# Kernel optimization log

Hardware: AMD Instinct MI355X
Metric: run time of the kernel (lower is better)

## Reference

```python
import jax, jax.numpy as jnp
import numpy as np

B, S, D, H, F = 2, 2048, 1024, 16, 4096
HD = D // H
EPS = 1e-5


def _layernorm(x, g, b):
    mu = jnp.mean(x, axis=-1, keepdims=True)
    var = jnp.var(x, axis=-1, keepdims=True)
    return (x - mu) * jax.lax.rsqrt(var + EPS) * g + b


def setup_inputs() -> dict:
    key = jax.random.key(0)
    ks = jax.random.split(key, 10)
    sd = 0.02
    return {
        "src": jax.random.normal(ks[0], (B, S, D), jnp.float32),
        "qkv_w": jax.random.normal(ks[1], (3 * D, D), jnp.float32) * sd,
        "qkv_b": jnp.zeros((3 * D,), jnp.float32),
        "out_w": jax.random.normal(ks[2], (D, D), jnp.float32) * sd,
        "out_b": jnp.zeros((D,), jnp.float32),
        "ffn_w1": jax.random.normal(ks[3], (F, D), jnp.float32) * sd,
        "ffn_b1": jnp.zeros((F,), jnp.float32),
        "ffn_w2": jax.random.normal(ks[4], (D, F), jnp.float32) * sd,
        "ffn_b2": jnp.zeros((D,), jnp.float32),
        "ln1_g": jnp.ones((D,), jnp.float32),
        "ln1_b": jnp.zeros((D,), jnp.float32),
        "ln2_g": jnp.ones((D,), jnp.float32),
        "ln2_b": jnp.zeros((D,), jnp.float32),
    }


def reference(src, qkv_w, qkv_b, out_w, out_b, ffn_w1, ffn_b1, ffn_w2, ffn_b2,
              ln1_g, ln1_b, ln2_g, ln2_b):
    # --- Multi-head self-attention (post-norm, dropout=identity in eval) ---
    qkv = src @ qkv_w.T + qkv_b                        # [B,S,3D]
    qkv = qkv.reshape(B, S, H, 3 * HD).transpose(0, 2, 1, 3)  # [B,H,S,3hd]
    q, k, v = jnp.split(qkv, 3, axis=-1)               # each [B,H,S,hd]
    scores = jnp.einsum('bhqd,bhkd->bhqk', q, k) / np.sqrt(HD).astype(np.float32)
    attn = jax.nn.softmax(scores, axis=-1)
    ctx = jnp.einsum('bhqk,bhkd->bhqd', attn, v)       # [B,H,S,hd]
    ctx = ctx.transpose(0, 2, 1, 3).reshape(B, S, D)
    mha_out = ctx @ out_w.T + out_b
    agg = _layernorm(src + mha_out, ln1_g, ln1_b)
    # --- FFN: Linear -> ReLU -> Linear ---
    h = jax.nn.relu(agg @ ffn_w1.T + ffn_b1)
    ffn_out = h @ ffn_w2.T + ffn_b2
    return _layernorm(agg + ffn_out, ln2_g, ln2_b)
```

## Files before the change

### kernel.cpp

```cpp
#include <hip/hip_runtime.h>


typedef unsigned short u16;
typedef unsigned int u32;
typedef __attribute__((ext_vector_type(8))) __bf16 bf16x8;
typedef __attribute__((ext_vector_type(4))) float f32x4;
typedef __attribute__((ext_vector_type(4))) short s16x4;
typedef __attribute__((ext_vector_type(2))) u32 u32x2;

__device__ __forceinline__ u16 f2bf(float f) {
  u32 u = __float_as_uint(f);
  u += 0x7fffu + ((u >> 16) & 1u);
  return (u16)(u >> 16);
}

__device__ __forceinline__ float bf2f(u16 h) {
  return __uint_as_float((u32)h << 16);
}

__device__ __forceinline__ u32 pk_bf_trunc(float a, float b) {
  return (__float_as_uint(a) >> 16) | (__float_as_uint(b) & 0xffff0000u);
}

__device__ __forceinline__ float exp2_fast(float x) {
  float t = __builtin_fmaf(x, 8388608.0f, 1064992506.0f);
  return __int_as_float((int)t);
}

__device__ __forceinline__ void async16(const void* g, void* l) {
  __builtin_amdgcn_global_load_lds((__attribute__((address_space(1))) void*)g,
                                   (__attribute__((address_space(3))) void*)l,
                                   16, 0, 0);
}

__device__ __forceinline__ f32x4 mfma16(bf16x8 a, bf16x8 b, f32x4 c) {
  return __builtin_amdgcn_mfma_f32_16x16x32_bf16(a, b, c, 0, 0, 0);
}

__device__ __forceinline__ f32x4 mfma_pv(s16x4 a, s16x4 b, f32x4 c) {
#if __has_builtin(__builtin_amdgcn_mfma_f32_16x16x16bf16_1k)
  return __builtin_amdgcn_mfma_f32_16x16x16bf16_1k(a, b, c, 0, 0, 0);
#else
  f32x4 d;
  asm("v_mfma_f32_16x16x16_bf16 %0, %1, %2, %3" : "=v"(d) : "v"(a), "v"(b), "v"(c));
  return d;
#endif
}

__global__ __launch_bounds__(256)
void cvt_all(const float* __restrict__ qkv_w, const float* __restrict__ out_w,
             const float* __restrict__ f1, const float* __restrict__ f2,
             const float* __restrict__ src,
             u16* __restrict__ o_qkv, u16* __restrict__ o_out,
             u16* __restrict__ o_f1, u16* __restrict__ o_f2,
             u16* __restrict__ o_src) {
  int b = blockIdx.x;
  const float* in;
  u16* out;
  int lb, ob;
  if (b < 3072) {
    int h = b / 192, c = b - h * 192;
    ob = (c < 64) ? h * 64 + c : (c < 128) ? 1024 + h * 64 + (c - 64)
                                           : 2048 + h * 64 + (c - 128);
    in = qkv_w; out = o_qkv; lb = b;
  }
  else if (b < 4096)  { in = out_w; out = o_out; lb = b - 3072;  ob = lb; }
  else if (b < 8192)  { in = f1;    out = o_f1;  lb = b - 4096;  ob = lb; }
  else if (b < 12288) { in = f2;    out = o_f2;  lb = b - 8192;  ob = lb; }
  else                { in = src;   out = o_src; lb = b - 12288; ob = lb; }
  int i = lb * 256 + threadIdx.x;
  int o = ob * 256 + threadIdx.x;
  float4 v = ((const float4*)in)[i];
  ushort4 ov;
  ov.x = f2bf(v.x); ov.y = f2bf(v.y); ov.z = f2bf(v.z); ov.w = f2bf(v.w);
  ((ushort4*)out)[o] = ov;
}

template <int MODE, int SPLIT>
__global__ __launch_bounds__(256)
void gemm_bt(const u16* __restrict__ A, const u16* __restrict__ W,
             const float* __restrict__ bias,
             u16* __restrict__ outb,
             u16* __restrict__ qo, u16* __restrict__ ko, u16* __restrict__ vto,
             int M, int N, int K) {
  __shared__ u16 As[128 * 64];
  __shared__ u16 Bs[128 * 64];
  const int lane = threadIdx.x & 63;
  const int wave = threadIdx.x >> 6;
  const int lrow = lane & 15;
  const int lq = lane >> 4;
  const int tm = blockIdx.x * 128;
  const int tn = blockIdx.y * 128;
  const int wm = (wave >> 1) * 64;
  const int wn = (wave & 1) * 64;
  const int kc = K / SPLIT;
  const int kbeg = blockIdx.z * kc;
  f32x4 acc[4][4] = {};

  for (int k0 = kbeg; k0 < kbeg + kc; k0 += 64) {
#pragma unroll
    for (int c = 0; c < 4; ++c) {
      int chunk = wave * 256 + c * 64 + lane;
      int row = chunk >> 3;
      int sc = chunk & 7;
      int cc = sc ^ (row & 7);
      u16* la = As + (size_t)(wave * 256 + c * 64) * 8;
      u16* lb = Bs + (size_t)(wave * 256 + c * 64) * 8;
      async16(A + (size_t)(tm + row) * K + (k0 + cc * 8), la);
      async16(W + (size_t)(tn + row) * K + (k0 + cc * 8), lb);
    }
    __syncthreads();
#pragma unroll
    for (int h = 0; h < 2; ++h) {
      bf16x8 a_frag[4], b_frag[4];
#pragma unroll
      for (int i = 0; i < 4; ++i) {
        int row = wm + i * 16 + lrow;
        int sc = (h * 4 + lq) ^ (row & 7);
        a_frag[i] = *(const bf16x8*)(As + row * 64 + sc * 8);
      }
#pragma unroll
      for (int j = 0; j < 4; ++j) {
        int row = wn + j * 16 + lrow;
        int sc = (h * 4 + lq) ^ (row & 7);
        b_frag[j] = *(const bf16x8*)(Bs + row * 64 + sc * 8);
      }
#pragma unroll
      for (int i = 0; i < 4; ++i)
#pragma unroll
        for (int j = 0; j < 4; ++j)
          acc[i][j] = mfma16(a_frag[i], b_frag[j], acc[i][j]);
    }
    __syncthreads();
  }

  u16* outp = outb;
  if constexpr (MODE == 0) outp += (size_t)blockIdx.z * M * N;

#pragma unroll
  for (int i = 0; i < 4; ++i) {
#pragma unroll
    for (int j = 0; j < 4; ++j) {
      int col = tn + wn + j * 16 + lrow;
      float bv = (SPLIT == 1 || blockIdx.z == 0) ? bias[col] : 0.f;
#pragma unroll
      for (int r = 0; r < 4; ++r) {
        int row = tm + wm + i * 16 + lq * 4 + r;
        float v = acc[i][j][r] + bv;
        if constexpr (MODE == 0) {
          outp[(size_t)row * N + col] = f2bf(v);
        } else {
          outp[(size_t)row * N + col] = f2bf(fmaxf(v, 0.f));
        }
      }
    }
  }
}

template <int MODE, int SPLIT>
__global__ __launch_bounds__(512, 2)
void gemm8p(const u16* __restrict__ A, const u16* __restrict__ W,
            const float* __restrict__ bias, u16* __restrict__ outb,
            u16* __restrict__ qo, u16* __restrict__ ko, u16* __restrict__ vto,
            int N, int Kfull) {
  extern __shared__ u16 lds[];
  constexpr int NTK = 16;
  constexpr int NG = NTK / 2;
  u16* As = lds;
  u16* Bs = lds + 32768;
  const int tid = threadIdx.x;
  const int lane = tid & 63;
  const int wave = tid >> 6;
  const int lrow = lane & 15;
  const int lq = lane >> 4;
  const int wm = wave >> 2;
  const int wn = wave & 3;
  const int kbeg = blockIdx.y * 1024;

  const int nwg = gridDim.x;
  const int wg = blockIdx.x;
  const int swz = (wg & 7) * (nwg >> 3) + (wg >> 3);
  const int tm = (swz & 15) * 256;
  const int tn = (swz >> 4) * 256;

  auto stage = [&](const u16* __restrict__ T, int trow0, int kt, int rbase,
                   u16* base) {
#pragma unroll
    for (int it = 0; it < 2; ++it) {
      int c = it * 512 + tid;
      int row = c >> 3, sc = c & 7, cc = sc ^ (row & 7);
      async16(T + (size_t)(trow0 + rbase + row) * Kfull + kbeg + kt * 64 + cc * 8,
              base + rbase * 64 + (it * 512 + wave * 64) * 8);
    }
  };
  auto ldA = [&](int buf, int m, int h) {
    int row = wm * 128 + m * 16 + lrow;
    int sc = (h * 4 + lq) ^ (row & 7);
    return *(const bf16x8*)(As + buf * 16384 + row * 64 + sc * 8);
  };
  auto ldB = [&](int buf, int n, int h) {
    int row = wn * 64 + n * 16 + lrow;
    int sc = (h * 4 + lq) ^ (row & 7);
    return *(const bf16x8*)(Bs + buf * 16384 + row * 64 + sc * 8);
  };

  f32x4 acc[8][4] = {};
  bf16x8 a[4][2], b[4][2];

  stage(A, tm, 0, 0, As);
  stage(A, tm, 0, 128, As);
  stage(W, tn, 0, 0, Bs);
  stage(W, tn, 0, 128, Bs);
  stage(W, tn, 1, 0, Bs + 16384);
  stage(A, tm, 1, 0, As + 16384);
  asm volatile("s_waitcnt vmcnt(4)" ::: "memory");
  __builtin_amdgcn_s_barrier();

  for (int g = 0; g < NG; ++g) {
    const int t = 2 * g;
    const int t1k = t + 1;
    const int t2k = (t + 2 < NTK) ? t + 2 : NTK - 1;
    const int t3k = (t + 3 < NTK) ? t + 3 : NTK - 1;

#pragma unroll
    for (int m = 0; m < 4; ++m) { a[m][0] = ldA(0, m, 0); a[m][1] = ldA(0, m, 1); }
#pragma unroll
    for (int n = 0; n < 2; ++n) { b[n][0] = ldB(0, n, 0); b[n][1] = ldB(0, n, 1); }
    stage(A, tm, t1k, 128, As + 16384);
    __builtin_amdgcn_s_barrier();
    asm volatile("s_waitcnt lgkmcnt(0)" ::: "memory");
    __builtin_amdgcn_s_setprio(1);
#pragma unroll
    for (int m = 0; m < 4; ++m)
#pragma unroll
      for (int n = 0; n < 2; ++n) {
        acc[m][n] = mfma16(a[m][0], b[n][0], acc[m][n]);
        acc[m][n] = mfma16(a[m][1], b[n][1], acc[m][n]);
      }
    __builtin_amdgcn_s_setprio(0);
    __builtin_amdgcn_s_barrier();

#pragma unroll
    for (int n = 0; n < 2; ++n) { b[2 + n][0] = ldB(0, 2 + n, 0); b[2 + n][1] = ldB(0, 2 + n, 1); }
    stage(W, tn, t1k, 128, Bs + 16384);
    __builtin_amdgcn_s_barrier();
    asm volatile("s_waitcnt lgkmcnt(0)" ::: "memory");
    __builtin_amdgcn_s_setprio(1);
#pragma unroll
    for (int m = 0; m < 4; ++m)
#pragma unroll
      for (int n = 0; n < 2; ++n) {
        acc[m][2 + n] = mfma16(a[m][0], b[2 + n][0], acc[m][2 + n]);
        acc[m][2 + n] = mfma16(a[m][1], b[2 + n][1], acc[m][2 + n]);
      }
    __builtin_amdgcn_s_setprio(0);
    __builtin_amdgcn_s_barrier();

#pragma unroll
    for (int m = 0; m < 4; ++m) { a[m][0] = ldA(0, 4 + m, 0); a[m][1] = ldA(0, 4 + m, 1); }
    stage(W, tn, t2k, 0, Bs);
    __builtin_amdgcn_s_barrier();
    asm volatile("s_waitcnt lgkmcnt(0)" ::: "memory");
    __builtin_amdgcn_s_setprio(1);
#pragma unroll
    for (int m = 0; m < 4; ++m)
#pragma unroll
      for (int n = 0; n < 2; ++n) {
        acc[4 + m][n] = mfma16(a[m][0], b[n][0], acc[4 + m][n]);
        acc[4 + m][n] = mfma16(a[m][1], b[n][1], acc[4 + m][n]);
      }
    __builtin_amdgcn_s_setprio(0);
    __builtin_amdgcn_s_barrier();

    stage(A, tm, t2k, 0, As);
    asm volatile("s_waitcnt vmcnt(4)" ::: "memory");
    __builtin_amdgcn_s_barrier();
    __builtin_amdgcn_s_setprio(1);
#pragma unroll
    for (int m = 0; m < 4; ++m)
#pragma unroll
      for (int n = 0; n < 2; ++n) {
        acc[4 + m][2 + n] = mfma16(a[m][0], b[2 + n][0], acc[4 + m][2 + n]);
        acc[4 + m][2 + n] = mfma16(a[m][1], b[2 + n][1], acc[4 + m][2 + n]);
      }
    __builtin_amdgcn_s_setprio(0);
    __builtin_amdgcn_s_barrier();

#pragma unroll
    for (int m = 0; m < 4; ++m) { a[m][0] = ldA(1, m, 0); a[m][1] = ldA(1, m, 1); }
#pragma unroll
    for (int n = 0; n < 2; ++n) { b[n][0] = ldB(1, n, 0); b[n][1] = ldB(1, n, 1); }
    stage(A, tm, t2k, 128, As);
    __builtin_amdgcn_s_barrier();
    asm volatile("s_waitcnt lgkmcnt(0)" ::: "memory");
    __builtin_amdgcn_s_setprio(1);
#pragma unroll
    for (int m = 0; m < 4; ++m)
#pragma unroll
      for (int n = 0; n < 2; ++n) {
        acc[m][n] = mfma16(a[m][0], b[n][0], acc[m][n]);
        acc[m][n] = mfma16(a[m][1], b[n][1], acc[m][n]);
      }
    __builtin_amdgcn_s_setprio(0);
    __builtin_amdgcn_s_barrier();

#pragma unroll
    for (int n = 0; n < 2; ++n) { b[2 + n][0] = ldB(1, 2 + n, 0); b[2 + n][1] = ldB(1, 2 + n, 1); }
    stage(W, tn, t2k, 128, Bs);
    __builtin_amdgcn_s_barrier();
    asm volatile("s_waitcnt lgkmcnt(0)" ::: "memory");
    __builtin_amdgcn_s_setprio(1);
#pragma unroll
    for (int m = 0; m < 4; ++m)
#pragma unroll
      for (int n = 0; n < 2; ++n) {
        acc[m][2 + n] = mfma16(a[m][0], b[2 + n][0], acc[m][2 + n]);
        acc[m][2 + n] = mfma16(a[m][1], b[2 + n][1], acc[m][2 + n]);
      }
    __builtin_amdgcn_s_setprio(0);
    __builtin_amdgcn_s_barrier();

#pragma unroll
    for (int m = 0; m < 4; ++m) { a[m][0] = ldA(1, 4 + m, 0); a[m][1] = ldA(1, 4 + m, 1); }
    stage(W, tn, t3k, 0, Bs + 16384);
    __builtin_amdgcn_s_barrier();
    asm volatile("s_waitcnt lgkmcnt(0)" ::: "memory");
    __builtin_amdgcn_s_setprio(1);
#pragma unroll
    for (int m = 0; m < 4; ++m)
#pragma unroll
      for (int n = 0; n < 2; ++n) {
        acc[4 + m][n] = mfma16(a[m][0], b[n][0], acc[4 + m][n]);
        acc[4 + m][n] = mfma16(a[m][1], b[n][1], acc[4 + m][n]);
      }
    __builtin_amdgcn_s_setprio(0);
    __builtin_amdgcn_s_barrier();

    stage(A, tm, t3k, 0, As + 16384);
    asm volatile("s_waitcnt vmcnt(4)" ::: "memory");
    __builtin_amdgcn_s_barrier();
    __builtin_amdgcn_s_setprio(1);
#pragma unroll
    for (int m = 0; m < 4; ++m)
#pragma unroll
      for (int n = 0; n < 2; ++n) {
        acc[4 + m][2 + n] = mfma16(a[m][0], b[2 + n][0], acc[4 + m][2 + n]);
        acc[4 + m][2 + n] = mfma16(a[m][1], b[2 + n][1], acc[4 + m][2 + n]);
      }
    __builtin_amdgcn_s_setprio(0);
    __builtin_amdgcn_s_barrier();
  }
  asm volatile("s_waitcnt vmcnt(0)" ::: "memory");

  if constexpr (MODE == 0) {
    u16* outp = outb + (size_t)blockIdx.y * 4096 * N;
#pragma unroll
    for (int m = 0; m < 8; ++m)
#pragma unroll
      for (int n = 0; n < 4; ++n) {
        int col = tn + wn * 64 + n * 16 + lrow;
        float bv = (SPLIT == 1 || blockIdx.y == 0) ? bias[col] : 0.f;
#pragma unroll
        for (int r = 0; r < 4; ++r) {
          int row = tm + wm * 128 + m * 16 + lq * 4 + r;
          outp[(size_t)row * N + col] = f2bf(acc[m][n][r] + bv);
        }
      }
  } else if constexpr (MODE == 1) {
#pragma unroll
    for (int m = 0; m < 8; ++m)
#pragma unroll
      for (int n = 0; n < 4; ++n) {
        int col = tn + wn * 64 + n * 16 + lrow;
        float bv = bias[col];
#pragma unroll
        for (int r = 0; r < 4; ++r) {
          int row = tm + wm * 128 + m * 16 + lq * 4 + r;
          outb[(size_t)row * N + col] = f2bf(fmaxf(acc[m][n][r] + bv, 0.f));
        }
      }
  } else {
    const int type = tn >> 10;
    if (type < 2) {
      u16* dst = (type == 0) ? qo : ko;
      const float scale = (type == 0) ? 0.1803368801f : 1.f;
#pragma unroll
      for (int n = 0; n < 4; ++n) {
        int idx = (tn & 1023) + wn * 64 + n * 16 + lrow;
        int hh = idx >> 6, c = idx & 63;
        float bv = bias[hh * 192 + type * 64 + c];
#pragma unroll
        for (int m = 0; m < 8; ++m) {
#pragma unroll
          for (int r = 0; r < 4; ++r) {
            int row = tm + wm * 128 + m * 16 + lq * 4 + r;
            int bb = row >> 11, s = row & 2047;
            dst[(((size_t)(bb * 16 + hh) * 2048 + s) << 6) + c] =
                f2bf((acc[m][n][r] + bv) * scale);
          }
        }
      }
    } else {
#pragma unroll
      for (int n = 0; n < 4; ++n) {
        int idx = (tn & 1023) + wn * 64 + n * 16 + lrow;
        int hh = idx >> 6, c = idx & 63;
        float bv = bias[hh * 192 + 128 + c];
#pragma unroll
        for (int m = 0; m < 8; ++m) {
          int row0 = tm + wm * 128 + m * 16 + lq * 4;
          int bb = row0 >> 11, s0 = row0 & 2047;
          ushort4 pk;
          pk.x = f2bf(acc[m][n][0] + bv);
          pk.y = f2bf(acc[m][n][1] + bv);
          pk.z = f2bf(acc[m][n][2] + bv);
          pk.w = f2bf(acc[m][n][3] + bv);
          *(ushort4*)(vto + (((size_t)(bb * 16 + hh) * 64 + c) << 11) + s0) = pk;
        }
      }
    }
  }
}

__global__ __launch_bounds__(512)
void attn_kernel(const u16* __restrict__ Q, const u16* __restrict__ K,
                 const u16* __restrict__ Vt,
                 u16* __restrict__ o_part, float* __restrict__ l_part) {
  extern __shared__ u16 smem[];
  u16* Ks = smem;
  u16* Vs = smem + 16384;
  const int tid = threadIdx.x;
  const int lane = tid & 63;
  const int wave = tid >> 6;
  const int wq = wave & 3;
  const int role = wave >> 2;
  const int lrow = lane & 15;
  const int q = lane >> 4;
  const int bh = blockIdx.x & 31;
  const int qb = (blockIdx.x >> 5) & 7;
  const int kvh = blockIdx.x >> 8;
  const u16* Qp = Q + ((size_t)bh * 2048 + qb * 256) * 64;
  const u16* Kp = K + (size_t)bh * 2048 * 64;
  const u16* Vp = Vt + (size_t)bh * 64 * 2048;

  bf16x8 qf[2][2];
#pragma unroll
  for (int h2 = 0; h2 < 2; ++h2)
#pragma unroll
    for (int kk = 0; kk < 2; ++kk)
      qf[h2][kk] = *(const bf16x8*)(Qp + (h2 * 128 + wave * 16 + lrow) * 64 +
                                    kk * 32 + q * 8);

  const s16x4 ones = {(short)0x3F80, (short)0x3F80, (short)0x3F80, (short)0x3F80};
  f32x4 oacc[2][4] = {};
  f32x4 lacc[2] = {};

  auto stage = [&](int kb, int buf) {
    if (role == 0) {
#pragma unroll
      for (int t = 0; t < 4; ++t) {
        int c = wq * 256 + t * 64 + lane;
        int row = c >> 3, sc = c & 7;
        int cc = sc ^ (row & 7);
        async16(Kp + (size_t)(kb * 128 + row) * 64 + cc * 8,
                Ks + buf * 8192 + (size_t)(wq * 256 + t * 64) * 8);
      }
    } else {
#pragma unroll
      for (int t = 0; t < 4; ++t) {
        int c = wq * 256 + t * 64 + lane;
        int row = c >> 4, sc = c & 15;
        int cc = sc ^ (row & 7);
        async16(Vp + (size_t)row * 2048 + kb * 128 + cc * 8,
                Vs + buf * 8192 + (size_t)(wq * 256 + t * 64) * 8);
      }
    }
  };

  const int kb0 = kvh * 8;
  stage(kb0, 0);
  asm volatile("s_waitcnt vmcnt(0)" ::: "memory");
  __builtin_amdgcn_s_barrier();

  for (int i = 0; i < 8; ++i) {
    const int buf = i & 1;
    if (i < 7) stage(kb0 + i + 1, buf ^ 1);
    const u16* Kb = Ks + buf * 8192;
    const u16* Vb = Vs + buf * 8192;

#pragma unroll
    for (int h2 = 0; h2 < 2; ++h2) {
      f32x4 sacc[8] = {};
#pragma unroll
      for (int j = 0; j < 8; ++j) {
#pragma unroll
        for (int kk = 0; kk < 2; ++kk) {
          int row = j * 16 + lrow;
          int sc = (kk * 4 + q) ^ (row & 7);
          bf16x8 kf = *(const bf16x8*)(Kb + row * 64 + sc * 8);
          sacc[j] = mfma16(kf, qf[h2][kk], sacc[j]);
        }
      }

      s16x4 pa[8];
#pragma unroll
      for (int j = 0; j < 8; ++j) {
        float p0 = exp2_fast(sacc[j][0]);
        float p1 = exp2_fast(sacc[j][1]);
        float p2 = exp2_fast(sacc[j][2]);
        float p3 = exp2_fast(sacc[j][3]);
        u32x2 pw;
        pw.x = pk_bf_trunc(p0, p1);
        pw.y = pk_bf_trunc(p2, p3);
        pa[j] = __builtin_bit_cast(s16x4, pw);
      }

#pragma unroll
      for (int j = 0; j < 8; ++j) {
        lacc[h2] = mfma_pv(pa[j], ones, lacc[h2]);
#pragma unroll
        for (int jn = 0; jn < 4; ++jn) {
          int row = jn * 16 + lrow;
          int sc = (j * 2 + (q >> 1)) ^ (row & 7);
          s16x4 vb = *(const s16x4*)(Vb + row * 128 + sc * 8 + (q & 1) * 4);
          oacc[h2][jn] = mfma_pv(pa[j], vb, oacc[h2][jn]);
        }
      }
    }

    if (i < 7) {
      asm volatile("s_waitcnt vmcnt(0)" ::: "memory");
      __builtin_amdgcn_s_barrier();
    }
  }

  const int b = bh >> 4, h = bh & 15;
  u16* op = o_part + (size_t)kvh * 4096 * 1024;
  float* lp = l_part + kvh * 65536 + bh * 2048;
#pragma unroll
  for (int h2 = 0; h2 < 2; ++h2) {
#pragma unroll
    for (int r = 0; r < 4; ++r) {
      int s = qb * 256 + h2 * 128 + wave * 16 + q * 4 + r;
      if (lrow == 0) lp[s] = lacc[h2][r];
      size_t base = ((size_t)(b * 2048 + s)) * 1024 + h * 64;
#pragma unroll
      for (int jn = 0; jn < 4; ++jn)
        op[base + jn * 16 + lrow] = f2bf(oacc[h2][jn][r]);
    }
  }
}

__global__ __launch_bounds__(256)
void attn_combine(const u16* __restrict__ o_part, const float* __restrict__ l_part,
                  u16* __restrict__ ctx) {
  const int t = blockIdx.x;
  const int tid = threadIdx.x;
  __shared__ float linv[16];
  if (tid < 16) {
    int b = t >> 11, s = t & 2047;
    int bh = b * 16 + tid;
    linv[tid] = 1.f / (l_part[bh * 2048 + s] + l_part[65536 + bh * 2048 + s]);
  }
  __syncthreads();
  size_t base = (size_t)t * 1024;
  ushort4 a = ((const ushort4*)(o_part + base))[tid];
  ushort4 c = ((const ushort4*)(o_part + 4096ull * 1024 + base))[tid];
  float li = linv[tid >> 4];
  ushort4 o;
  o.x = f2bf((bf2f(a.x) + bf2f(c.x)) * li);
  o.y = f2bf((bf2f(a.y) + bf2f(c.y)) * li);
  o.z = f2bf((bf2f(a.z) + bf2f(c.z)) * li);
  o.w = f2bf((bf2f(a.w) + bf2f(c.w)) * li);
  ((ushort4*)(ctx + base))[tid] = o;
}

template <int P>
__global__ __launch_bounds__(256)
void ln_kernel(const float* __restrict__ x1, const u16* __restrict__ x2,
               const float* __restrict__ g, const float* __restrict__ bb,
               float* __restrict__ outf, u16* __restrict__ outb) {
  const int t = blockIdx.x;
  const int tid = threadIdx.x;
  const int lane = tid & 63, wave = tid >> 6;
  const size_t base = (size_t)t * 1024;
  const size_t pstride = 4096ull * 1024;
  float v[4];
  float s = 0.f, s2 = 0.f;
#pragma unroll
  for (int e = 0; e < 4; ++e) {
    int i = tid + e * 256;
    float x = x1[base + i];
#pragma unroll
    for (int p = 0; p < P; ++p) x += bf2f(x2[p * pstride + base + i]);
    v[e] = x;
    s += x;
    s2 += x * x;
  }
#pragma unroll
  for (int d = 1; d < 64; d <<= 1) {
    s += __shfl_xor(s, d);
    s2 += __shfl_xor(s2, d);
  }
  __shared__ float red[8];
  if (lane == 0) { red[wave] = s; red[4 + wave] = s2; }
  __syncthreads();
  s = red[0] + red[1] + red[2] + red[3];
  s2 = red[4] + red[5] + red[6] + red[7];
  float mean = s * (1.f / 1024.f);
  float var = s2 * (1.f / 1024.f) - mean * mean;
  float rstd = rsqrtf(var + 1e-5f);
#pragma unroll
  for (int e = 0; e < 4; ++e) {
    int i = tid + e * 256;
    float y = (v[e] - mean) * rstd * g[i] + bb[i];
    outf[base + i] = y;
    if (outb) outb[base + i] = f2bf(y);
  }
}

extern "C" void kernel_launch(void* const* d_in, const int* in_sizes, int n_in,
                              void* d_out, int out_size, void* d_ws, size_t ws_size,
                              hipStream_t stream) {
  const float* src    = (const float*)d_in[0];
  const float* qkv_w  = (const float*)d_in[1];
  const float* qkv_b  = (const float*)d_in[2];
  const float* out_w  = (const float*)d_in[3];
  const float* out_b  = (const float*)d_in[4];
  const float* ffn_w1 = (const float*)d_in[5];
  const float* ffn_b1 = (const float*)d_in[6];
  const float* ffn_w2 = (const float*)d_in[7];
  const float* ffn_b2 = (const float*)d_in[8];
  const float* ln1_g  = (const float*)d_in[9];
  const float* ln1_b  = (const float*)d_in[10];
  const float* ln2_g  = (const float*)d_in[11];
  const float* ln2_b  = (const float*)d_in[12];

  char* ws = (char*)d_ws;
  size_t off = 0;
  auto alloc = [&](size_t bytes) -> void* {
    void* p = ws + off;
    off += (bytes + 255) & ~(size_t)255;
    return p;
  };
  u16* wqkv = (u16*)alloc(3072ull * 1024 * 2);
  u16* wout = (u16*)alloc(1024ull * 1024 * 2);
  u16* wf1  = (u16*)alloc(4096ull * 1024 * 2);
  u16* wf2  = (u16*)alloc(1024ull * 4096 * 2);
  u16* srcb = (u16*)alloc(4096ull * 1024 * 2);
  u16* qb_  = (u16*)alloc(32ull * 2048 * 64 * 2);
  u16* kb_  = (u16*)alloc(32ull * 2048 * 64 * 2);
  u16* vtb  = (u16*)alloc(32ull * 64 * 2048 * 2);
  u16* opart = (u16*)alloc(2ull * 4096 * 1024 * 2);
  float* lpart = (float*)alloc(2ull * 65536 * 4);
  u16* ctxb = (u16*)alloc(4096ull * 1024 * 2);
  u16* mha  = (u16*)alloc(4ull * 4096 * 1024 * 2);
  float* aggf = (float*)alloc(4096ull * 1024 * 4);
  u16* aggb = (u16*)alloc(4096ull * 1024 * 2);
  u16* hb   = (u16*)alloc(4096ull * 4096 * 2);
  u16* ffnf = (u16*)alloc(4ull * 4096 * 1024 * 2);

  static bool attr_done = false;
  if (!attr_done) {
    auto* kq = gemm8p<2, 1>;
    auto* kf = gemm8p<1, 1>;
    auto* k2 = gemm8p<0, 4>;
    hipFuncSetAttribute(reinterpret_cast<const void*>(kq),
                        hipFuncAttributeMaxDynamicSharedMemorySize, 131072);
    hipFuncSetAttribute(reinterpret_cast<const void*>(kf),
                        hipFuncAttributeMaxDynamicSharedMemorySize, 131072);
    hipFuncSetAttribute(reinterpret_cast<const void*>(k2),
                        hipFuncAttributeMaxDynamicSharedMemorySize, 131072);
    hipFuncSetAttribute(reinterpret_cast<const void*>(attn_kernel),
                        hipFuncAttributeMaxDynamicSharedMemorySize, 65536);
    attr_done = true;
  }

  cvt_all<<<16384, 256, 0, stream>>>(qkv_w, out_w, ffn_w1, ffn_w2, src,
                                     wqkv, wout, wf1, wf2, srcb);

  gemm8p<2, 1><<<dim3(192, 1), 512, 131072, stream>>>(srcb, wqkv, qkv_b, nullptr,
                                                      qb_, kb_, vtb, 3072, 1024);
  attn_kernel<<<512, 512, 65536, stream>>>(qb_, kb_, vtb, opart, lpart);
  attn_combine<<<4096, 256, 0, stream>>>(opart, lpart, ctxb);
  gemm_bt<0, 4><<<dim3(32, 8, 4), 256, 0, stream>>>(ctxb, wout, out_b, mha,
                                                    nullptr, nullptr, nullptr, 4096, 1024, 1024);
  ln_kernel<4><<<4096, 256, 0, stream>>>(src, mha, ln1_g, ln1_b, aggf, aggb);
  gemm8p<1, 1><<<dim3(256, 1), 512, 131072, stream>>>(aggb, wf1, ffn_b1, hb,
                                                      nullptr, nullptr, nullptr, 4096, 1024);
  gemm8p<0, 4><<<dim3(64, 4), 512, 131072, stream>>>(hb, wf2, ffn_b2, ffnf,
                                                     nullptr, nullptr, nullptr, 1024, 4096);
  ln_kernel<4><<<4096, 256, 0, stream>>>(aggf, ffnf, ln2_g, ln2_b, (float*)d_out, nullptr);
}
```

Measured before the change: 362.8 us.

## Transpose V epilogue through LDS and share V fragment loads across query halves

In the QKV GEMM epilogue, the transposed V output is now staged through a per-wave LDS tile so each lane writes 16-byte contiguous chunks along the sequence dimension, replacing scattered 8-byte stores. A barrier is added before the epilogue so the LDS can be reused safely. In the attention kernel, the P fragments for both query halves are computed first, and each V fragment read from LDS then feeds both halves' PV MFMAs, halving V LDS reads. The cost is higher register pressure from holding both P arrays, plus extra LDS waits in the epilogue.

```diff
diff --git a/kernel.cpp b/kernel.cpp
--- a/kernel.cpp
+++ b/kernel.cpp
@@ -351,6 +351,7 @@
     __builtin_amdgcn_s_barrier();
   }
   asm volatile("s_waitcnt vmcnt(0)" ::: "memory");
+  __builtin_amdgcn_s_barrier();
 
   if constexpr (MODE == 0) {
     u16* outp = outb + (size_t)blockIdx.y * 4096 * N;
@@ -401,21 +402,36 @@
         }
       }
     } else {
-#pragma unroll
-      for (int n = 0; n < 4; ++n) {
-        int idx = (tn & 1023) + wn * 64 + n * 16 + lrow;
-        int hh = idx >> 6, c = idx & 63;
-        float bv = bias[hh * 192 + 128 + c];
-#pragma unroll
-        for (int m = 0; m < 8; ++m) {
-          int row0 = tm + wm * 128 + m * 16 + lq * 4;
-          int bb = row0 >> 11, s0 = row0 & 2047;
-          ushort4 pk;
-          pk.x = f2bf(acc[m][n][0] + bv);
-          pk.y = f2bf(acc[m][n][1] + bv);
-          pk.z = f2bf(acc[m][n][2] + bv);
-          pk.w = f2bf(acc[m][n][3] + bv);
-          *(ushort4*)(vto + (((size_t)(bb * 16 + hh) * 64 + c) << 11) + s0) = pk;
+      u16* T = lds + wave * 640;
+      const int bb = tm >> 11;
+      const int s_base = (tm & 2047) + wm * 128;
+      const int idxl = lane & 15, sg = lane >> 4;
+      const int idx2 = (tn & 1023) + wn * 64 + idxl;
+#pragma unroll
+      for (int p = 0; p < 4; ++p) {
+#pragma unroll
+        for (int n = 0; n < 4; ++n) {
+          int idx = (tn & 1023) + wn * 64 + n * 16 + lrow;
+          int hh = idx >> 6, c = idx & 63;
+          float bv = bias[hh * 192 + 128 + c];
+          ushort4 lo, hi;
+          lo.x = f2bf(acc[2 * p][n][0] + bv);
+          lo.y = f2bf(acc[2 * p][n][1] + bv);
+          lo.z = f2bf(acc[2 * p][n][2] + bv);
+          lo.w = f2bf(acc[2 * p][n][3] + bv);
+          hi.x = f2bf(acc[2 * p + 1][n][0] + bv);
+          hi.y = f2bf(acc[2 * p + 1][n][1] + bv);
+          hi.z = f2bf(acc[2 * p + 1][n][2] + bv);
+          hi.w = f2bf(acc[2 * p + 1][n][3] + bv);
+          *(ushort4*)(T + lrow * 40 + lq * 4) = lo;
+          *(ushort4*)(T + lrow * 40 + 16 + lq * 4) = hi;
+          asm volatile("s_waitcnt lgkmcnt(0)" ::: "memory");
+          int i2 = idx2 + n * 16;
+          int hh2 = i2 >> 6, c2 = i2 & 63;
+          uint4 v = *(const uint4*)(T + idxl * 40 + sg * 8);
+          *(uint4*)(vto + (((size_t)(bb * 16 + hh2) * 64 + c2) << 11)
+                        + s_base + p * 32 + sg * 8) = v;
+          asm volatile("s_waitcnt lgkmcnt(0)" ::: "memory");
         }
       }
     }
@@ -488,6 +504,7 @@
     const u16* Kb = Ks + buf * 8192;
     const u16* Vb = Vs + buf * 8192;
 
+    s16x4 pa2[2][8];
 #pragma unroll
     for (int h2 = 0; h2 < 2; ++h2) {
       f32x4 sacc[8] = {};
@@ -501,8 +518,6 @@
           sacc[j] = mfma16(kf, qf[h2][kk], sacc[j]);
         }
       }
-
-      s16x4 pa[8];
 #pragma unroll
       for (int j = 0; j < 8; ++j) {
         float p0 = exp2_fast(sacc[j][0]);
@@ -512,19 +527,21 @@
         u32x2 pw;
         pw.x = pk_bf_trunc(p0, p1);
         pw.y = pk_bf_trunc(p2, p3);
-        pa[j] = __builtin_bit_cast(s16x4, pw);
-      }
-
-#pragma unroll
-      for (int j = 0; j < 8; ++j) {
-        lacc[h2] = mfma_pv(pa[j], ones, lacc[h2]);
-#pragma unroll
-        for (int jn = 0; jn < 4; ++jn) {
-          int row = jn * 16 + lrow;
-          int sc = (j * 2 + (q >> 1)) ^ (row & 7);
-          s16x4 vb = *(const s16x4*)(Vb + row * 128 + sc * 8 + (q & 1) * 4);
-          oacc[h2][jn] = mfma_pv(pa[j], vb, oacc[h2][jn]);
-        }
+        pa2[h2][j] = __builtin_bit_cast(s16x4, pw);
+      }
+    }
+
+#pragma unroll
+    for (int j = 0; j < 8; ++j) {
+      lacc[0] = mfma_pv(pa2[0][j], ones, lacc[0]);
+      lacc[1] = mfma_pv(pa2[1][j], ones, lacc[1]);
+#pragma unroll
+      for (int jn = 0; jn < 4; ++jn) {
+        int row = jn * 16 + lrow;
+        int sc = (j * 2 + (q >> 1)) ^ (row & 7);
+        s16x4 vb = *(const s16x4*)(Vb + row * 128 + sc * 8 + (q & 1) * 4);
+        oacc[0][jn] = mfma_pv(pa2[0][j], vb, oacc[0][jn]);
+        oacc[1][jn] = mfma_pv(pa2[1][j], vb, oacc[1][jn]);
       }
     }
 
```

After: 361.4 us. Within noise of the previous version (-0.4%).
